# Optimization experiments

Hardware: AMD Instinct MI355X
Metric: run time of the kernel (lower is better)

Reference implementation:

```python
import jax, jax.numpy as jnp
import numpy as np

B, T, D = 4, 2048, 1024
H, HD = 16, 64  # n_heads, head_dim; H*HD == D

def setup_inputs() -> dict:
    key = jax.random.key(0)
    ks = jax.random.split(key, 9)
    s = 1.0 / np.sqrt(D)
    return {
        "x": jax.random.normal(ks[0], (B, T, D), dtype=jnp.float32),
        "Wq": jax.random.normal(ks[1], (D, D), dtype=jnp.float32) * s,
        "bq": jnp.zeros((D,), dtype=jnp.float32),
        "Wk": jax.random.normal(ks[2], (D, D), dtype=jnp.float32) * s,
        "bk": jnp.zeros((D,), dtype=jnp.float32),
        "Wv": jax.random.normal(ks[3], (D, D), dtype=jnp.float32) * s,
        "bv": jnp.zeros((D,), dtype=jnp.float32),
        "Wo": jax.random.normal(ks[4], (D, D), dtype=jnp.float32) * s,
        "bo": jnp.zeros((D,), dtype=jnp.float32),
    }

def reference(x, Wq, bq, Wk, bk, Wv, bv, Wo, bo):
    # Linear(in,out): y = x @ W.T + b (weights stored [out,in])
    q = (jnp.einsum('btd,ed->bte', x, Wq) + bq).reshape(B, T, H, HD).transpose(0, 2, 1, 3)
    k = (jnp.einsum('btd,ed->bte', x, Wk) + bk).reshape(B, T, H, HD).transpose(0, 2, 1, 3)
    v = (jnp.einsum('btd,ed->bte', x, Wv) + bv).reshape(B, T, H, HD).transpose(0, 2, 1, 3)
    scale = jnp.sqrt(jnp.asarray(HD, dtype=x.dtype))
    attn = jnp.einsum('bhqd,bhkd->bhqk', q, k) / scale  # [B,H,T,T]
    attn = jax.nn.softmax(attn, axis=-1)
    out = jnp.einsum('bhqk,bhkd->bhqd', attn, v)
    out = out.transpose(0, 2, 1, 3).reshape(B, T, H * HD)
    return jnp.einsum('bte,de->btd', out, Wo) + bo
```

## Files before the change

### kernel.cpp

```cpp
#include <hip/hip_runtime.h>
#include <hip/hip_bf16.h>

#define B_ 4
#define T_ 2048
#define D_ 1024
#define H_ 16
#define HD_ 64
#define M_ (B_ * T_)

typedef __attribute__((ext_vector_type(8))) short   s16x8;
typedef __attribute__((ext_vector_type(4))) short   s16x4;
typedef __attribute__((ext_vector_type(4))) float   f32x4;
typedef __attribute__((ext_vector_type(4))) float   fvec4;
typedef __attribute__((ext_vector_type(4))) unsigned short u16x4;

union U4 { u16x4 v; unsigned int w[2]; };
union P8 { s16x8 v; unsigned int w[4]; };

__device__ inline unsigned short f2bf(float f) {
    unsigned int u = __float_as_uint(f);
    return (unsigned short)((u + 0x7fffu + ((u >> 16) & 1u)) >> 16);
}

__device__ inline unsigned int pk_bf16(float a, float b) {
    unsigned int r;
    asm("v_cvt_pk_bf16_f32 %0, %1, %2" : "=v"(r) : "v"(a), "v"(b));
    return r;
}

__device__ inline f32x4 mfma32(s16x8 a, s16x8 b, f32x4 c) {
    return __builtin_amdgcn_mfma_f32_16x16x32_bf16(a, b, c, 0, 0, 0);
}

__device__ inline void gld16(const unsigned short* g, unsigned short* l) {
    __builtin_amdgcn_global_load_lds(
        (const __attribute__((address_space(1))) unsigned int*)g,
        (__attribute__((address_space(3))) unsigned int*)l, 16, 0, 0);
}

__global__ void cvt_all(const float* __restrict__ x,
                        const float* __restrict__ wq, const float* __restrict__ wk,
                        const float* __restrict__ wv, const float* __restrict__ wo,
                        unsigned short* __restrict__ xb, unsigned short* __restrict__ wcat) {
    const int bid = blockIdx.x;
    const float* src; unsigned short* dst; int off;
    if (bid < 8192)       { src = x;  dst = xb;                  off = bid; }
    else if (bid < 9216)  { src = wq; dst = wcat;                off = bid - 8192; }
    else if (bid < 10240) { src = wk; dst = wcat + 1 * 1048576;  off = bid - 9216; }
    else if (bid < 11264) { src = wv; dst = wcat + 2 * 1048576;  off = bid - 10240; }
    else                  { src = wo; dst = wcat + 3 * 1048576;  off = bid - 11264; }
    int i = off * 1024 + threadIdx.x * 4;
    fvec4 v = *(const fvec4*)(src + i);
    U4 o;
    o.w[0] = pk_bf16(v[0], v[1]);
    o.w[1] = pk_bf16(v[2], v[3]);
    *(u16x4*)(dst + i) = o.v;
}

#define GEMM_BODY(A_, W_, SWAPPED_)                                                \
    __shared__ __align__(16) unsigned short As[2][128 * 32];                       \
    __shared__ __align__(16) unsigned short Bs[2][128 * 32];                       \
    const int tid = threadIdx.x;                                                   \
    const int wave = tid >> 6, lane = tid & 63;                                    \
    const int quad = lane >> 4, l16 = lane & 15;                                   \
    const int wr = (wave >> 1) * 64, wc = (wave & 1) * 64;                         \
    f32x4 acc[4][4] = {};                                                          \
    {                                                                              \
        for (int i = 0; i < 2; ++i) {                                              \
            int idx = tid + i * 256;                                               \
            int row = idx >> 2, c8 = (idx & 3) * 8;                                \
            gld16(A_ + (size_t)(m0 + row) * 1024 + c8, As[0] + idx * 8);           \
            gld16(W_ + (size_t)(n0 + row) * 1024 + c8, Bs[0] + idx * 8);           \
        }                                                                          \
    }                                                                              \
    for (int c = 0; c < 32; ++c) {                                                 \
        __syncthreads();                                                           \
        if (c + 1 < 32) {                                                          \
            int kn = (c + 1) * 32, nb = (c + 1) & 1;                               \
            for (int i = 0; i < 2; ++i) {                                          \
                int idx = tid + i * 256;                                           \
                int row = idx >> 2, c8 = (idx & 3) * 8;                            \
                gld16(A_ + (size_t)(m0 + row) * 1024 + kn + c8, As[nb] + idx * 8); \
                gld16(W_ + (size_t)(n0 + row) * 1024 + kn + c8, Bs[nb] + idx * 8); \
            }                                                                      \
        }                                                                          \
        const unsigned short* Ac = As[c & 1];                                      \
        const unsigned short* Bc = Bs[c & 1];                                      \
        s16x8 af[4], bfr[4];                                                       \
        for (int i = 0; i < 4; ++i)                                                \
            af[i] = *(const s16x8*)(Ac + (wr + i * 16 + l16) * 32 + quad * 8);     \
        for (int j = 0; j < 4; ++j)                                                \
            bfr[j] = *(const s16x8*)(Bc + (wc + j * 16 + l16) * 32 + quad * 8);    \
        if (SWAPPED_) {                                                            \
            for (int i = 0; i < 4; ++i)                                            \
                for (int j = 0; j < 4; ++j)                                        \
                    acc[i][j] = mfma32(bfr[j], af[i], acc[i][j]);                  \
        } else {                                                                   \
            for (int i = 0; i < 4; ++i)                                            \
                for (int j = 0; j < 4; ++j)                                        \
                    acc[i][j] = mfma32(af[i], bfr[j], acc[i][j]);                  \
        }                                                                          \
    }

__global__ __launch_bounds__(256) void gemm_qkv(
    const unsigned short* __restrict__ A, const unsigned short* __restrict__ Wcat,
    const float* __restrict__ bq, const float* __restrict__ bk, const float* __restrict__ bv,
    unsigned short* __restrict__ Qb, unsigned short* __restrict__ Kb,
    unsigned short* __restrict__ Vt, float qscale) {
    const int proj = blockIdx.y >> 3;
    const int m0 = blockIdx.x * 128, n0 = (blockIdx.y & 7) * 128;
    const unsigned short* W = Wcat + (size_t)proj * 1048576;
    const float* bias = proj == 0 ? bq : (proj == 1 ? bk : bv);
    const bool swapped = (proj != 2);

    GEMM_BODY(A, W, swapped)

    if (proj == 2) {
        for (int i = 0; i < 4; ++i) {
            int mbase = m0 + wr + i * 16 + quad * 4;
            int b = mbase >> 11, t = mbase & (T_ - 1);
            int tp = (t & ~31) | (((t >> 2) & 3) << 3) | (((t >> 4) & 1) << 2);
            for (int j = 0; j < 4; ++j) {
                int n = n0 + wc + j * 16 + l16;
                float bi = bias[n];
                int h = n >> 6, hd = n & 63;
                U4 o;
                o.w[0] = pk_bf16(acc[i][j][0] + bi, acc[i][j][1] + bi);
                o.w[1] = pk_bf16(acc[i][j][2] + bi, acc[i][j][3] + bi);
                *(u16x4*)(Vt + ((size_t)(b * H_ + h) * HD_ + hd) * T_ + tp) = o.v;
            }
        }
    } else {
        const float scale = (proj == 0) ? qscale : 1.0f;
        unsigned short* outp = (proj == 0) ? Qb : Kb;
        for (int i = 0; i < 4; ++i) {
            int t = m0 + wr + i * 16 + l16;
            int b = t >> 11, tt = t & (T_ - 1);
            for (int j = 0; j < 4; ++j) {
                int nb = n0 + wc + j * 16 + quad * 4;
                fvec4 bi = *(const fvec4*)(bias + nb);
                int h = nb >> 6, hd = nb & 63;
                float v0 = (acc[i][j][0] + bi[0]) * scale;
                float v1 = (acc[i][j][1] + bi[1]) * scale;
                float v2 = (acc[i][j][2] + bi[2]) * scale;
                float v3 = (acc[i][j][3] + bi[3]) * scale;
                U4 o;
                o.w[0] = pk_bf16(v0, v1);
                o.w[1] = pk_bf16(v2, v3);
                *(u16x4*)(outp + ((size_t)(b * H_ + h) * T_ + tt) * HD_ + hd) = o.v;
            }
        }
    }
}

__global__ __launch_bounds__(256) void gemm_o(
    const unsigned short* __restrict__ A, const unsigned short* __restrict__ W,
    const float* __restrict__ bias, float* __restrict__ out) {
    const int m0 = blockIdx.x * 128, n0 = blockIdx.y * 128;

    GEMM_BODY(A, W, true)

    for (int i = 0; i < 4; ++i) {
        int m = m0 + wr + i * 16 + l16;
        for (int j = 0; j < 4; ++j) {
            int nb = n0 + wc + j * 16 + quad * 4;
            fvec4 bi = *(const fvec4*)(bias + nb);
            fvec4 o = acc[i][j] + bi;
            *(fvec4*)(out + (size_t)m * D_ + nb) = o;
        }
    }
}

__global__ __launch_bounds__(256) void attn(
    const unsigned short* __restrict__ Qb, const unsigned short* __restrict__ Kb,
    const unsigned short* __restrict__ Vt, unsigned short* __restrict__ Ob) {
    __shared__ __align__(16) unsigned short Ks[2 * 4096];
    __shared__ __align__(16) unsigned short Vs[2 * 4096];

    const int tid = threadIdx.x;
    const int wave = tid >> 6, lane = tid & 63;
    const int quad = lane >> 4, l16 = lane & 15;

    const int flat = blockIdx.y * 16 + blockIdx.x;
    const int wid  = (flat & 7) * 128 + (flat >> 3);
    const int qblk = wid & 15, bh = wid >> 4;
    const int b = bh >> 4, h = bh & 15;
    const int q0 = qblk * 128 + wave * 32;

    const unsigned short* Qp = Qb + (size_t)bh * T_ * HD_;
    const unsigned short* Kp = Kb + (size_t)bh * T_ * HD_;
    const unsigned short* Vp = Vt + (size_t)bh * HD_ * T_;

    s16x8 qf[2][2];
    for (int qt = 0; qt < 2; ++qt)
        for (int ds = 0; ds < 2; ++ds)
            qf[qt][ds] = *(const s16x8*)(Qp + (size_t)(q0 + qt * 16 + l16) * HD_ + ds * 32 + quad * 8);

    f32x4 accO[2][4] = {};
    f32x4 accL[2] = {};
    const f32x4 fzero = {0.f, 0.f, 0.f, 0.f};

    const s16x8 ones = {0x3F80, 0x3F80, 0x3F80, 0x3F80,
                        0x3F80, 0x3F80, 0x3F80, 0x3F80};

    const int r0 = tid >> 3,           cg0 = (tid & 7) ^ (r0 & 7);
    const int r1 = (tid + 256) >> 3,   cg1 = (tid & 7) ^ (r1 & 7);

    const unsigned short* kp0 = Kp + (size_t)r0 * HD_ + cg0 * 8;
    const unsigned short* kp1 = Kp + (size_t)r1 * HD_ + cg1 * 8;
    const unsigned short* vp0 = Vp + (size_t)r0 * T_ + cg0 * 8;
    const unsigned short* vp1 = Vp + (size_t)r1 * T_ + cg1 * 8;

    const int xk   = quad ^ (l16 & 7);
    const int kro  = l16 * 64 + xk * 8;
    const int kro1 = l16 * 64 + (xk ^ 4) * 8;
    const int vro0 = l16 * 64 + ((quad)     ^ (l16 & 7)) * 8;
    const int vro1 = l16 * 64 + ((4 + quad) ^ (l16 & 7)) * 8;

    gld16(kp0, Ks + tid * 8);  gld16(kp1, Ks + tid * 8 + 2048);
    gld16(vp0, Vs + tid * 8);  gld16(vp1, Vs + tid * 8 + 2048);
    kp0 += 64 * HD_; kp1 += 64 * HD_; vp0 += 64; vp1 += 64;

    for (int c = 0; c < T_ / 64; ++c) {
        __syncthreads();

        if (c + 1 < T_ / 64) {
            unsigned short* dK = Ks + ((c + 1) & 1) * 4096 + tid * 8;
            unsigned short* dV = Vs + ((c + 1) & 1) * 4096 + tid * 8;
            gld16(kp0, dK);  gld16(kp1, dK + 2048);
            gld16(vp0, dV);  gld16(vp1, dV + 2048);
            kp0 += 64 * HD_; kp1 += 64 * HD_; vp0 += 64; vp1 += 64;
        }

        const unsigned short* Kc = Ks + (c & 1) * 4096;
        const unsigned short* Vc = Vs + (c & 1) * 4096;

        f32x4 st[2][4];
        __builtin_amdgcn_s_setprio(1);
        for (int kt = 0; kt < 4; ++kt) {
            s16x8 kf0 = *(const s16x8*)(Kc + kt * 1024 + kro);
            s16x8 kf1 = *(const s16x8*)(Kc + kt * 1024 + kro1);
            st[0][kt] = mfma32(kf0, qf[0][0], fzero);
            st[0][kt] = mfma32(kf1, qf[0][1], st[0][kt]);
            st[1][kt] = mfma32(kf0, qf[1][0], fzero);
            st[1][kt] = mfma32(kf1, qf[1][1], st[1][kt]);
        }
        __builtin_amdgcn_s_setprio(0);

        s16x8 pf[2][2];
        for (int qt = 0; qt < 2; ++qt)
            for (int u = 0; u < 2; ++u) {
                P8 pk;
                for (int kk = 0; kk < 2; ++kk) {
                    f32x4 s = st[qt][2 * u + kk];
                    float p0 = __builtin_amdgcn_exp2f(s[0]);
                    float p1 = __builtin_amdgcn_exp2f(s[1]);
                    float p2 = __builtin_amdgcn_exp2f(s[2]);
                    float p3 = __builtin_amdgcn_exp2f(s[3]);
                    pk.w[2 * kk]     = pk_bf16(p0, p1);
                    pk.w[2 * kk + 1] = pk_bf16(p2, p3);
                }
                pf[qt][u] = pk.v;
            }

        __builtin_amdgcn_s_setprio(1);
        accL[0] = mfma32(ones, pf[0][0], accL[0]);
        accL[1] = mfma32(ones, pf[1][0], accL[1]);
        for (int dt = 0; dt < 4; ++dt) {
            s16x8 vf = *(const s16x8*)(Vc + vro0 + dt * 1024);
            accO[0][dt] = mfma32(vf, pf[0][0], accO[0][dt]);
            accO[1][dt] = mfma32(vf, pf[1][0], accO[1][dt]);
        }
        accL[0] = mfma32(ones, pf[0][1], accL[0]);
        accL[1] = mfma32(ones, pf[1][1], accL[1]);
        for (int dt = 0; dt < 4; ++dt) {
            s16x8 vf = *(const s16x8*)(Vc + vro1 + dt * 1024);
            accO[0][dt] = mfma32(vf, pf[0][1], accO[0][dt]);
            accO[1][dt] = mfma32(vf, pf[1][1], accO[1][dt]);
        }
        __builtin_amdgcn_s_setprio(0);
    }

    for (int qt = 0; qt < 2; ++qt) {
        float inv = 1.f / accL[qt][0];
        int t = q0 + qt * 16 + l16;
        for (int dt = 0; dt < 4; ++dt) {
            U4 o;
            o.w[0] = pk_bf16(accO[qt][dt][0] * inv, accO[qt][dt][1] * inv);
            o.w[1] = pk_bf16(accO[qt][dt][2] * inv, accO[qt][dt][3] * inv);
            *(u16x4*)(Ob + ((size_t)b * T_ + t) * D_ + h * 64 + dt * 16 + quad * 4) = o.v;
        }
    }
}

extern "C" void kernel_launch(void* const* d_in, const int* in_sizes, int n_in,
                              void* d_out, int out_size, void* d_ws, size_t ws_size,
                              hipStream_t stream) {
    const float* x  = (const float*)d_in[0];
    const float* Wq = (const float*)d_in[1];
    const float* bq = (const float*)d_in[2];
    const float* Wk = (const float*)d_in[3];
    const float* bk = (const float*)d_in[4];
    const float* Wv = (const float*)d_in[5];
    const float* bv = (const float*)d_in[6];
    const float* Wo = (const float*)d_in[7];
    const float* bo = (const float*)d_in[8];
    float* out = (float*)d_out;

    const size_t SZ = (size_t)M_ * D_ * sizeof(unsigned short);
    unsigned short* xb   = (unsigned short*)d_ws;
    unsigned short* Qb   = (unsigned short*)((char*)d_ws + 1 * SZ);
    unsigned short* Kb   = (unsigned short*)((char*)d_ws + 2 * SZ);
    unsigned short* Vbt  = (unsigned short*)((char*)d_ws + 3 * SZ);
    unsigned short* Wcat = (unsigned short*)((char*)d_ws + 4 * SZ);
    unsigned short* Ob   = xb;

    const float qscale = 1.4426950408889634f / 8.0f;

    dim3 blk(256);
    cvt_all<<<dim3(12288), blk, 0, stream>>>(x, Wq, Wk, Wv, Wo, xb, Wcat);
    gemm_qkv<<<dim3(M_ / 128, 24), blk, 0, stream>>>(xb, Wcat, bq, bk, bv, Qb, Kb, Vbt, qscale);
    attn<<<dim3(T_ / 128, B_ * H_), blk, 0, stream>>>(Qb, Kb, Vbt, Ob);
    gemm_o<<<dim3(M_ / 128, D_ / 128), blk, 0, stream>>>(Ob, Wcat + 3 * 1048576, bo, out);
}
```

Before: 307.0 us.

## Triple-buffer GEMM LDS staging with XOR swizzle and remapped block order

The GEMM body moves from double to triple buffering. Loads are issued two k-steps ahead, and a manual vmcnt wait plus a raw s_barrier replace __syncthreads, so global loads can overlap more of the MFMA work. The LDS column chunk is XOR-swizzled by row to reduce bank conflicts on the fragment reads. Both GEMMs now use a flattened 1D grid with an m-tile remapping, which changes which tiles run concurrently and may improve L2 locality. In exchange, LDS use per block rises by half, which could lower occupancy, and the hand-counted vmcnt must stay correct.

```diff
diff --git a/kernel.cpp b/kernel.cpp
--- a/kernel.cpp
+++ b/kernel.cpp
@@ -57,40 +57,41 @@
     *(u16x4*)(dst + i) = o.v;
 }
 
+#define STAGE_(A_, W_, kn_, buf_)                                                  \
+    for (int i = 0; i < 2; ++i) {                                                  \
+        int idx = tid + i * 256;                                                   \
+        int row = idx >> 2, c8 = ((idx & 3) ^ ((idx >> 3) & 3)) * 8;               \
+        gld16(A_ + (size_t)(m0 + row) * 1024 + (kn_) + c8, As[buf_] + idx * 8);    \
+        gld16(W_ + (size_t)(n0 + row) * 1024 + (kn_) + c8, Bs[buf_] + idx * 8);    \
+    }
+
 #define GEMM_BODY(A_, W_, SWAPPED_)                                                \
-    __shared__ __align__(16) unsigned short As[2][128 * 32];                       \
-    __shared__ __align__(16) unsigned short Bs[2][128 * 32];                       \
+    __shared__ __align__(16) unsigned short As[3][128 * 32];                       \
+    __shared__ __align__(16) unsigned short Bs[3][128 * 32];                       \
     const int tid = threadIdx.x;                                                   \
     const int wave = tid >> 6, lane = tid & 63;                                    \
     const int quad = lane >> 4, l16 = lane & 15;                                   \
     const int wr = (wave >> 1) * 64, wc = (wave & 1) * 64;                         \
+    const int sxo = (quad ^ ((l16 >> 1) & 3)) * 8;                                 \
     f32x4 acc[4][4] = {};                                                          \
-    {                                                                              \
-        for (int i = 0; i < 2; ++i) {                                              \
-            int idx = tid + i * 256;                                               \
-            int row = idx >> 2, c8 = (idx & 3) * 8;                                \
-            gld16(A_ + (size_t)(m0 + row) * 1024 + c8, As[0] + idx * 8);           \
-            gld16(W_ + (size_t)(n0 + row) * 1024 + c8, Bs[0] + idx * 8);           \
+    STAGE_(A_, W_, 0, 0)                                                           \
+    STAGE_(A_, W_, 32, 1)                                                          \
+    int rb = 0;                                                                    \
+    for (int c = 0; c < 32; ++c) {                                                 \
+        if (c + 1 < 32) { asm volatile("s_waitcnt vmcnt(4)" ::: "memory"); }       \
+        else            { asm volatile("s_waitcnt vmcnt(0)" ::: "memory"); }       \
+        __builtin_amdgcn_s_barrier();                                              \
+        if (c + 2 < 32) {                                                          \
+            int wb = rb >= 1 ? rb - 1 : 2;                                         \
+            STAGE_(A_, W_, (c + 2) * 32, wb)                                       \
         }                                                                          \
-    }                                                                              \
-    for (int c = 0; c < 32; ++c) {                                                 \
-        __syncthreads();                                                           \
-        if (c + 1 < 32) {                                                          \
-            int kn = (c + 1) * 32, nb = (c + 1) & 1;                               \
-            for (int i = 0; i < 2; ++i) {                                          \
-                int idx = tid + i * 256;                                           \
-                int row = idx >> 2, c8 = (idx & 3) * 8;                            \
-                gld16(A_ + (size_t)(m0 + row) * 1024 + kn + c8, As[nb] + idx * 8); \
-                gld16(W_ + (size_t)(n0 + row) * 1024 + kn + c8, Bs[nb] + idx * 8); \
-            }                                                                      \
-        }                                                                          \
-        const unsigned short* Ac = As[c & 1];                                      \
-        const unsigned short* Bc = Bs[c & 1];                                      \
+        const unsigned short* Ac = As[rb];                                         \
+        const unsigned short* Bc = Bs[rb];                                         \
         s16x8 af[4], bfr[4];                                                       \
         for (int i = 0; i < 4; ++i)                                                \
-            af[i] = *(const s16x8*)(Ac + (wr + i * 16 + l16) * 32 + quad * 8);     \
+            af[i] = *(const s16x8*)(Ac + (wr + i * 16 + l16) * 32 + sxo);          \
         for (int j = 0; j < 4; ++j)                                                \
-            bfr[j] = *(const s16x8*)(Bc + (wc + j * 16 + l16) * 32 + quad * 8);    \
+            bfr[j] = *(const s16x8*)(Bc + (wc + j * 16 + l16) * 32 + sxo);         \
         if (SWAPPED_) {                                                            \
             for (int i = 0; i < 4; ++i)                                            \
                 for (int j = 0; j < 4; ++j)                                        \
@@ -100,6 +101,7 @@
                 for (int j = 0; j < 4; ++j)                                        \
                     acc[i][j] = mfma32(af[i], bfr[j], acc[i][j]);                  \
         }                                                                          \
+        rb = rb == 2 ? 0 : rb + 1;                                                 \
     }
 
 __global__ __launch_bounds__(256) void gemm_qkv(
@@ -107,8 +109,12 @@
     const float* __restrict__ bq, const float* __restrict__ bk, const float* __restrict__ bv,
     unsigned short* __restrict__ Qb, unsigned short* __restrict__ Kb,
     unsigned short* __restrict__ Vt, float qscale) {
-    const int proj = blockIdx.y >> 3;
-    const int m0 = blockIdx.x * 128, n0 = (blockIdx.y & 7) * 128;
+    const int flat = blockIdx.x;
+    const int j = flat >> 3;
+    const int mt = (flat & 7) * 8 + (j & 7);
+    const int y  = j >> 3;
+    const int proj = y >> 3;
+    const int m0 = mt * 128, n0 = (y & 7) * 128;
     const unsigned short* W = Wcat + (size_t)proj * 1048576;
     const float* bias = proj == 0 ? bq : (proj == 1 ? bk : bv);
     const bool swapped = (proj != 2);
@@ -120,13 +126,13 @@
             int mbase = m0 + wr + i * 16 + quad * 4;
             int b = mbase >> 11, t = mbase & (T_ - 1);
             int tp = (t & ~31) | (((t >> 2) & 3) << 3) | (((t >> 4) & 1) << 2);
-            for (int j = 0; j < 4; ++j) {
-                int n = n0 + wc + j * 16 + l16;
+            for (int jj = 0; jj < 4; ++jj) {
+                int n = n0 + wc + jj * 16 + l16;
                 float bi = bias[n];
                 int h = n >> 6, hd = n & 63;
                 U4 o;
-                o.w[0] = pk_bf16(acc[i][j][0] + bi, acc[i][j][1] + bi);
-                o.w[1] = pk_bf16(acc[i][j][2] + bi, acc[i][j][3] + bi);
+                o.w[0] = pk_bf16(acc[i][jj][0] + bi, acc[i][jj][1] + bi);
+                o.w[1] = pk_bf16(acc[i][jj][2] + bi, acc[i][jj][3] + bi);
                 *(u16x4*)(Vt + ((size_t)(b * H_ + h) * HD_ + hd) * T_ + tp) = o.v;
             }
         }
@@ -136,14 +142,14 @@
         for (int i = 0; i < 4; ++i) {
             int t = m0 + wr + i * 16 + l16;
             int b = t >> 11, tt = t & (T_ - 1);
-            for (int j = 0; j < 4; ++j) {
-                int nb = n0 + wc + j * 16 + quad * 4;
+            for (int jj = 0; jj < 4; ++jj) {
+                int nb = n0 + wc + jj * 16 + quad * 4;
                 fvec4 bi = *(const fvec4*)(bias + nb);
                 int h = nb >> 6, hd = nb & 63;
-                float v0 = (acc[i][j][0] + bi[0]) * scale;
-                float v1 = (acc[i][j][1] + bi[1]) * scale;
-                float v2 = (acc[i][j][2] + bi[2]) * scale;
-                float v3 = (acc[i][j][3] + bi[3]) * scale;
+                float v0 = (acc[i][jj][0] + bi[0]) * scale;
+                float v1 = (acc[i][jj][1] + bi[1]) * scale;
+                float v2 = (acc[i][jj][2] + bi[2]) * scale;
+                float v3 = (acc[i][jj][3] + bi[3]) * scale;
                 U4 o;
                 o.w[0] = pk_bf16(v0, v1);
                 o.w[1] = pk_bf16(v2, v3);
@@ -156,16 +162,19 @@
 __global__ __launch_bounds__(256) void gemm_o(
     const unsigned short* __restrict__ A, const unsigned short* __restrict__ W,
     const float* __restrict__ bias, float* __restrict__ out) {
-    const int m0 = blockIdx.x * 128, n0 = blockIdx.y * 128;
+    const int flat = blockIdx.x;
+    const int j = flat >> 3;
+    const int m0 = ((flat & 7) * 8 + (j & 7)) * 128;
+    const int n0 = (j >> 3) * 128;
 
     GEMM_BODY(A, W, true)
 
     for (int i = 0; i < 4; ++i) {
         int m = m0 + wr + i * 16 + l16;
-        for (int j = 0; j < 4; ++j) {
-            int nb = n0 + wc + j * 16 + quad * 4;
+        for (int jj = 0; jj < 4; ++jj) {
+            int nb = n0 + wc + jj * 16 + quad * 4;
             fvec4 bi = *(const fvec4*)(bias + nb);
-            fvec4 o = acc[i][j] + bi;
+            fvec4 o = acc[i][jj] + bi;
             *(fvec4*)(out + (size_t)m * D_ + nb) = o;
         }
     }
@@ -319,7 +328,7 @@
 
     dim3 blk(256);
     cvt_all<<<dim3(12288), blk, 0, stream>>>(x, Wq, Wk, Wv, Wo, xb, Wcat);
-    gemm_qkv<<<dim3(M_ / 128, 24), blk, 0, stream>>>(xb, Wcat, bq, bk, bv, Qb, Kb, Vbt, qscale);
+    gemm_qkv<<<dim3(1536), blk, 0, stream>>>(xb, Wcat, bq, bk, bv, Qb, Kb, Vbt, qscale);
     attn<<<dim3(T_ / 128, B_ * H_), blk, 0, stream>>>(Qb, Kb, Vbt, Ob);
-    gemm_o<<<dim3(M_ / 128, D_ / 128), blk, 0, stream>>>(Ob, Wcat + 3 * 1048576, bo, out);
-}
+    gemm_o<<<dim3(512), blk, 0, stream>>>(Ob, Wcat + 3 * 1048576, bo, out);
+}
```

Measured after the change: 303.7 us. About the same (-1.1%).
